# Performance work log

Hardware: AMD Instinct MI355X
Metric: run time of the kernel (lower is better)

Reference implementation:

```python
import jax, jax.numpy as jnp
import numpy as np

K = 5        # spline kernel_size per dim (dim=2 -> 25 kernel weights)
NPG = 75     # MNIST superpixel nodes per graph


def _spline_conv(x, src, dst, pseudo, emask, W, root, bias):
    """SplineConv, dim=2, kernel_size=5, degree=1 open splines, aggr='mean'.
    emask in {0,1} masks out coalesced-away (duplicate/self-loop) edges."""
    n = x.shape[0]
    v = jnp.clip(pseudo, 0.0, 1.0) * (K - 1)
    bot = jnp.clip(jnp.floor(v), 0, K - 2)
    frac = v - bot                                   # [E,2]
    bot = bot.astype(jnp.int32)
    xj = x[src] * emask[:, None]                     # [E,Fin] gathered source feats
    # aggregate-then-transform: acc[k,i,:] = sum over edges into i with basis k
    acc = jnp.zeros((K * K, n, x.shape[1]), x.dtype)
    for o0 in (0, 1):
        for o1 in (0, 1):
            w = (frac[:, 0] if o0 else 1.0 - frac[:, 0]) * (frac[:, 1] if o1 else 1.0 - frac[:, 1])
            kk = (bot[:, 0] + o0) + K * (bot[:, 1] + o1)
            acc = acc.at[kk, dst].add(w[:, None] * xj)
    out = jnp.einsum('knf,kfo->no', acc, W)
    deg = jax.ops.segment_sum(emask, dst, num_segments=n)
    return out / jnp.maximum(deg, 1.0)[:, None] + x @ root + bias


def _pool(x, pos, valid, batch, src, dst, emask, size, G, B):
    """voxel_grid + max_pool with static shapes: S=B*G*G clusters, masked."""
    S = B * G * G
    c = jnp.clip(jnp.floor(pos / size).astype(jnp.int32), 0, G - 1)
    cl = batch * (G * G) + c[:, 1] * G + c[:, 0]
    xm = jnp.where(valid[:, None] > 0, x, -1e30)
    px = jax.ops.segment_max(xm, cl, num_segments=S)
    cnt = jax.ops.segment_sum(valid, cl, num_segments=S)
    sval = (cnt > 0).astype(x.dtype)
    px = jnp.where(sval[:, None] > 0, px, 0.0)
    ppos = jax.ops.segment_sum(pos * valid[:, None], cl, num_segments=S) / jnp.maximum(cnt, 1.0)[:, None]
    nb = jnp.arange(S, dtype=jnp.int32) // (G * G)
    # remap edges to clusters; mask self loops and duplicates (= coalesce)
    nsrc, ndst = cl[src], cl[dst]
    m = (emask > 0) & (nsrc != ndst)
    a0 = jnp.where(m, nsrc, S)
    b0 = jnp.where(m, ndst, S)
    order = jnp.lexsort((b0, a0))
    a, b = a0[order], b0[order]
    first = jnp.concatenate([jnp.array([True]), (a[1:] != a[:-1]) | (b[1:] != b[:-1])])
    keep = jnp.zeros(src.shape[0], dtype=bool).at[order].set(first & (a < S))
    kf = keep.astype(x.dtype)
    # T.Cartesian(cat=False, norm=True): pseudo = (pos_src-pos_dst)/(2*max|.|)+0.5
    cart = ppos[nsrc] - ppos[ndst]
    amax = jnp.maximum(jnp.max(jnp.abs(cart) * kf[:, None]), 1e-12)
    pseudo = cart / (2.0 * amax) + 0.5
    return px, ppos, sval, nb, nsrc, ndst, kf, pseudo


def _forward(x, pos, src, dst, W1, r1, b1, W2, r2, b2, W3, r3, b3, fw1, fb1, fw2, fb2):
    N = x.shape[0]
    B = N // NPG
    batch = jnp.arange(N, dtype=jnp.int32) // NPG
    valid = jnp.ones((N,), x.dtype)
    emask = jnp.ones((src.shape[0],), x.dtype)
    cart = pos[src] - pos[dst]
    pseudo = cart / (2.0 * jnp.maximum(jnp.max(jnp.abs(cart)), 1e-12)) + 0.5
    x = jax.nn.elu(_spline_conv(x, src, dst, pseudo, emask, W1, r1, b1))
    x, pos, valid, batch, src, dst, emask, pseudo = _pool(x, pos, valid, batch, src, dst, emask, 5.0, 6, B)
    x = jax.nn.elu(_spline_conv(x, src, dst, pseudo, emask, W2, r2, b2))
    x, pos, valid, batch, src, dst, emask, pseudo = _pool(x, pos, valid, batch, src, dst, emask, 7.0, 5, B)
    x = jax.nn.elu(_spline_conv(x, src, dst, pseudo, emask, W3, r3, b3))
    # max_pool_x(cluster, x, batch, size=4): 2x2 voxel grid (size=14, end=27.99)
    c = jnp.clip(jnp.floor(pos / 14.0).astype(jnp.int32), 0, 1)
    cl = batch * 4 + c[:, 1] * 2 + c[:, 0]
    xm = jnp.where(valid[:, None] > 0, x, -1e30)
    px = jax.ops.segment_max(xm, cl, num_segments=B * 4)
    cnt = jax.ops.segment_sum(valid, cl, num_segments=B * 4)
    px = jnp.where((cnt > 0)[:, None], px, 0.0)
    h = jax.nn.elu(px.reshape(B, 4 * 64) @ fw1.T + fb1)
    logits = h @ fw2.T + fb2  # F.dropout is identity in eval mode
    return jax.nn.log_softmax(logits, axis=1)


def setup_inputs() -> dict:
    key = jax.random.key(0)
    ks = jax.random.split(key, 16)
    B, EPG = 1024, 1392
    N = B * NPG
    x = jax.random.normal(ks[0], (N, 1), jnp.float32)
    pos = jax.random.uniform(ks[1], (N, 2), jnp.float32) * 27.99
    s = jax.random.randint(ks[2], (B, EPG), 0, NPG)
    d = (s + 1 + jax.random.randint(ks[3], (B, EPG), 0, NPG - 1)) % NPG  # no self loops
    off = (jnp.arange(B, dtype=jnp.int32) * NPG)[:, None]
    src = (s + off).reshape(-1)
    dst = (d + off).reshape(-1)
    rn = lambda k, sh, sc: jax.random.normal(k, sh, jnp.float32) * sc
    return dict(x=x, pos=pos, src=src, dst=dst,
                W1=rn(ks[4], (25, 1, 32), 0.2), r1=rn(ks[5], (1, 32), 0.2), b1=jnp.zeros((32,), jnp.float32),
                W2=rn(ks[6], (25, 32, 64), 0.05), r2=rn(ks[7], (32, 64), 0.1), b2=jnp.zeros((64,), jnp.float32),
                W3=rn(ks[8], (25, 64, 64), 0.04), r3=rn(ks[9], (64, 64), 0.08), b3=jnp.zeros((64,), jnp.float32),
                fw1=rn(ks[10], (128, 256), 0.06), fb1=jnp.zeros((128,), jnp.float32),
                fw2=rn(ks[11], (10, 128), 0.09), fb2=jnp.zeros((10,), jnp.float32))


def reference(x, pos, src, dst, W1, r1, b1, W2, r2, b2, W3, r3, b3, fw1, fb1, fw2, fb2):
    return _forward(x, pos, src, dst, W1, r1, b1, W2, r2, b2, W3, r3, b3, fw1, fb1, fw2, fb2)
```

## Files before the change

kernel.cpp:

```cpp
#include <hip/hip_runtime.h>
#include <math.h>

#define NPG 75
#define KDIM 5

typedef _Float16 half8 __attribute__((ext_vector_type(8)));
typedef _Float16 half4 __attribute__((ext_vector_type(4)));
typedef float f32x4 __attribute__((ext_vector_type(4)));

__device__ __forceinline__ float eluf(float v){ return v > 0.f ? v : expf(v) - 1.f; }

__device__ __forceinline__ void atomAddF(float* p, float v){ unsafeAtomicAdd(p, v); }

__device__ __forceinline__ unsigned fenc(float f){
    unsigned u = __float_as_uint(f);
    return (u & 0x80000000u) ? ~u : (u | 0x80000000u);
}
__device__ __forceinline__ float fdec(unsigned u){
    return (u & 0x80000000u) ? __uint_as_float(u & 0x7FFFFFFFu) : __uint_as_float(~u);
}

__device__ __forceinline__ void fma25(float (&r)[25], const float (&wx)[5], const float (&wyx)[5]){
    #pragma unroll
    for (int b1 = 0; b1 < 5; b1++)
        #pragma unroll
        for (int b0 = 0; b0 < 5; b0++)
            asm("v_fmac_f32 %0, %1, %2" : "+v"(r[b1 * 5 + b0]) : "v"(wx[b0]), "v"(wyx[b1]));
}

__device__ __forceinline__ void spline2(float c0, float c1, float am, int* kks, float* wsp){
    float denom = 2.f * fmaxf(am, 1e-12f);
    float p0 = c0 / denom + 0.5f;
    float p1 = c1 / denom + 0.5f;
    p0 = fminf(fmaxf(p0, 0.f), 1.f) * 4.f;
    p1 = fminf(fmaxf(p1, 0.f), 1.f) * 4.f;
    float b0 = fminf(floorf(p0), 3.f);
    float b1 = fminf(floorf(p1), 3.f);
    float f0 = p0 - b0, f1 = p1 - b1;
    int i0 = (int)b0, i1 = (int)b1;
    wsp[0] = (1.f - f0) * (1.f - f1); kks[0] = i0     + KDIM *  i1;
    wsp[1] =        f0  * (1.f - f1); kks[1] = i0 + 1 + KDIM *  i1;
    wsp[2] = (1.f - f0) *        f1 ; kks[2] = i0     + KDIM * (i1 + 1);
    wsp[3] =        f0  *        f1 ; kks[3] = i0 + 1 + KDIM * (i1 + 1);
}

__global__ __launch_bounds__(256) void amax0_k(
        const float* __restrict__ pos, const int* __restrict__ src,
        const int* __restrict__ dst, int E4, unsigned* __restrict__ outbits){
    float cand = 0.f;
    for (int i = blockIdx.x * 256 + threadIdx.x; i < E4; i += gridDim.x * 256){
        int4 s4 = ((const int4*)src)[i];
        int4 d4 = ((const int4*)dst)[i];
        #pragma unroll
        for (int k = 0; k < 4; k++){
            int s = (&s4.x)[k], d = (&d4.x)[k];
            float c0 = pos[s*2]   - pos[d*2];
            float c1 = pos[s*2+1] - pos[d*2+1];
            cand = fmaxf(cand, fmaxf(fabsf(c0), fabsf(c1)));
        }
    }
    __shared__ float sm[256];
    sm[threadIdx.x] = cand; __syncthreads();
    for (int o = 128; o > 0; o >>= 1){
        if (threadIdx.x < o) sm[threadIdx.x] = fmaxf(sm[threadIdx.x], sm[threadIdx.x + o]);
        __syncthreads();
    }
    if (threadIdx.x == 0) atomicMax(outbits, __float_as_uint(sm[0]));
}

__global__ __launch_bounds__(512) void conv1dedup_k(
        const float* __restrict__ x, const float* __restrict__ pos,
        const int* __restrict__ src, const int* __restrict__ dst, int EPG,
        const unsigned* __restrict__ amaxp,
        const float* __restrict__ W1, const float* __restrict__ r1, const float* __restrict__ b1,
        float* __restrict__ px1, float* __restrict__ pp1, float* __restrict__ sv1,
        int* __restrict__ easrc, float2* __restrict__ ecart,
        int* __restrict__ rowptr2, int* __restrict__ kcnt, unsigned* __restrict__ amaxbits){
    __shared__ __align__(16) float acc[NPG * 28];
    __shared__ float deg[NPG];
    __shared__ float xl[NPG], p0l[NPG], p1l[NPG];
    __shared__ int   cli[NPG];
    __shared__ float W1s[800], r1s[32], b1s[32];
    __shared__ unsigned px[36 * 32];
    __shared__ float cnt[36], ps[72], ppS[72];
    __shared__ unsigned pm[36 * 36];
    __shared__ float degs[36];
    __shared__ int rs[37], cur[36];
    __shared__ float red[8];
    __shared__ unsigned short sdS[2048];

    const int b = blockIdx.x, t = threadIdx.x;
    const int lane = t & 63, wid = t >> 6;
    const int n0 = b * NPG, e0 = b * EPG;

    const float am = __uint_as_float(*amaxp);

    for (int i = t; i < NPG * 28; i += 512) acc[i] = 0.f;
    for (int i = t; i < 36 * 32; i += 512) px[i] = 0u;
    for (int i = t; i < 36 * 36; i += 512) pm[i] = 0xFFFFFFFFu;
    if (t < NPG) deg[t] = 0.f;
    if (t < 36){ cnt[t] = 0.f; degs[t] = 0.f; }
    if (t < 72) ps[t] = 0.f;
    for (int i = t; i < 800; i += 512) W1s[i] = W1[i];
    if (t < 32){ r1s[t] = r1[t]; b1s[t] = b1[t]; }
    if (t < NPG){
        float p0 = pos[(n0 + t) * 2], p1 = pos[(n0 + t) * 2 + 1];
        xl[t] = x[n0 + t]; p0l[t] = p0; p1l[t] = p1;
        int c0 = min(max((int)floorf(p0 / 5.f), 0), 5);
        int c1 = min(max((int)floorf(p1 / 5.f), 0), 5);
        cli[t] = c1 * 6 + c0;
    }
    __syncthreads();

    if (t < NPG){
        int c = cli[t];
        atomAddF(&cnt[c], 1.f);
        atomAddF(&ps[c*2],     p0l[t]);
        atomAddF(&ps[c*2 + 1], p1l[t]);
    }
    #pragma unroll 4
    for (int it = 0; it < 4; it++){
        int e = t + it * 512;
        if (e < EPG){
            int s = src[e0 + e] - n0;
            int d = dst[e0 + e] - n0;
            sdS[e] = (unsigned short)(s | (d << 8));
            float c0 = p0l[s] - p0l[d];
            float c1 = p1l[s] - p1l[d];
            int kks[4]; float wsp[4];
            spline2(c0, c1, am, kks, wsp);
            float xv = xl[s];
            #pragma unroll
            for (int c = 0; c < 4; c++) atomAddF(&acc[d*28 + kks[c]], wsp[c] * xv);
            atomAddF(&deg[d], 1.f);
        }
    }
    __syncthreads();

    if (t < 36){
        float c = cnt[t], m = fmaxf(c, 1.f);
        float q0 = ps[t*2] / m, q1 = ps[t*2 + 1] / m;
        ppS[t*2] = q0; ppS[t*2 + 1] = q1;
        pp1[(b*36 + t)*2]     = q0;
        pp1[(b*36 + t)*2 + 1] = q1;
        sv1[b*36 + t] = (c > 0.f) ? 1.f : 0.f;
    }
    {
        const int o = t & 31;
        float wreg[25];
        #pragma unroll
        for (int k = 0; k < 25; k++) wreg[k] = W1s[k * 32 + o];
        const float rro = r1s[o], bbo = b1s[o];
        const int ii = t >> 5;
        #pragma unroll
        for (int r = 0; r < 5; r++){
            int i = ii + r * 16;
            if (i < NPG){
                const float4* ar = (const float4*)(acc + i * 28);
                float s = 0.f;
                #pragma unroll
                for (int q = 0; q < 7; q++){
                    float4 aq = ar[q];
                    s += aq.x * wreg[q*4];
                    if (q*4 + 1 < 25) s += aq.y * wreg[q*4 + 1];
                    if (q*4 + 2 < 25) s += aq.z * wreg[q*4 + 2];
                    if (q*4 + 3 < 25) s += aq.w * wreg[q*4 + 3];
                }
                float v = s / fmaxf(deg[i], 1.f) + xl[i] * rro + bbo;
                v = eluf(v);
                atomicMax(&px[cli[i]*32 + o], fenc(v));
            }
        }
    }
    int lab[4];
    #pragma unroll 4
    for (int it = 0; it < 4; it++){
        int e = t + it * 512;
        lab[it] = 0;
        if (e < EPG){
            int sd = (int)sdS[e];
            int a  = cli[sd & 255];
            int bb = cli[sd >> 8];
            lab[it] = a | (bb << 8) | ((a != bb) ? 0x10000 : 0);
            if (a != bb) atomicMin(&pm[a * 36 + bb], (unsigned)e);
        }
    }
    __syncthreads();

    for (int idx = t; idx < 36 * 32; idx += 512){
        int s_ = idx >> 5;
        px1[(size_t)(b*36)*32 + idx] = (cnt[s_] > 0.f) ? fdec(px[idx]) : 0.f;
    }
    float cand = 0.f;
    unsigned keptM = 0;
    #pragma unroll 4
    for (int it = 0; it < 4; it++){
        int e = t + it * 512;
        int L = lab[it];
        if (L & 0x10000){
            int a = L & 255, bb = (L >> 8) & 255;
            if (pm[a * 36 + bb] == (unsigned)e){
                keptM |= 1u << it;
                atomAddF(&degs[bb], 1.f);
                float c0 = ppS[a*2]     - ppS[bb*2];
                float c1 = ppS[a*2 + 1] - ppS[bb*2 + 1];
                cand = fmaxf(cand, fmaxf(fabsf(c0), fabsf(c1)));
            }
        }
    }
    #pragma unroll
    for (int o = 1; o < 64; o <<= 1) cand = fmaxf(cand, __shfl_xor(cand, o, 64));
    if (lane == 0) red[wid] = cand;
    __syncthreads();
    if (t == 0){
        float m = red[0];
        #pragma unroll
        for (int i = 1; i < 8; i++) m = fmaxf(m, red[i]);
        atomicMax(amaxbits, __float_as_uint(m));
    }
    if (t < 64){
        int v = (t < 36) ? (int)degs[t] : 0;
        int incl = v;
        #pragma unroll
        for (int o = 1; o < 64; o <<= 1){
            int u = __shfl_up(incl, o, 64);
            if (t >= o) incl += u;
        }
        if (t == 0) rs[0] = 0;
        if (t < 36) rs[t + 1] = incl;
    }
    __syncthreads();
    if (t < 36){
        rowptr2[(b*36 + t)*2]     = e0 + rs[t];
        rowptr2[(b*36 + t)*2 + 1] = e0 + rs[t + 1];
        cur[t] = rs[t];
    }
    if (t == 0) kcnt[b] = rs[36];
    __syncthreads();
    #pragma unroll 4
    for (int it = 0; it < 4; it++){
        if (keptM & (1u << it)){
            int L = lab[it];
            int a = L & 255, bb = (L >> 8) & 255;
            int slot = atomicAdd(&cur[bb], 1);
            easrc[e0 + slot] = b*36 + a;
            ecart[e0 + slot] = make_float2(ppS[a*2] - ppS[bb*2], ppS[a*2 + 1] - ppS[bb*2 + 1]);
        }
    }
}

__global__ __launch_bounds__(1024) void dedup_pool_k(
        const int* __restrict__ easrc_in, const int* __restrict__ rowptr_in,
        const int* __restrict__ kcnt_in,
        const float* __restrict__ xin,
        const float* __restrict__ pp1, const float* __restrict__ sv1,
        int EPG,
        float* __restrict__ px2, float* __restrict__ pp2, float* __restrict__ sv2,
        int* __restrict__ easrc, float2* __restrict__ ecart,
        int* __restrict__ rowptr2, int* __restrict__ kcnt, unsigned* __restrict__ amaxbits){
    constexpr int GG = 25, NN = 36;
    __shared__ unsigned pm[GG * GG];
    __shared__ float degs[GG];
    __shared__ int rs[GG + 1];
    __shared__ int cur[GG];
    __shared__ float red[16];
    __shared__ int   clS[NN];
    __shared__ int   vld[NN];
    __shared__ int   rsS[NN + 1];
    __shared__ float ppS[2 * GG];
    __shared__ unsigned px[GG * 64];
    __shared__ float cnt[GG], ps[2 * GG];
    __shared__ unsigned short abS[1280];

    const int b = blockIdx.x, t = threadIdx.x;
    const int lane = t & 63, wid = t >> 6;
    const int e0 = b * EPG;
    const int cb25 = b * GG;
    const int nb36 = b * NN;

    for (int i = t; i < GG * GG; i += 1024) pm[i] = 0xFFFFFFFFu;
    for (int i = t; i < GG * 64; i += 1024) px[i] = 0u;
    if (t < GG){ degs[t] = 0.f; cnt[t] = 0.f; }
    if (t < 2 * GG) ps[t] = 0.f;
    if (t < NN){
        float v  = sv1[nb36 + t];
        float p0 = pp1[(nb36 + t)*2], p1 = pp1[(nb36 + t)*2 + 1];
        int c0 = min(max((int)floorf(p0 / 7.f), 0), 4);
        int c1 = min(max((int)floorf(p1 / 7.f), 0), 4);
        clS[t] = c1 * 5 + c0;
        vld[t] = (v > 0.f) ? 1 : 0;
        rsS[t] = rowptr_in[(nb36 + t)*2] - e0;
    }
    if (t == 0) rsS[NN] = kcnt_in[b];
    __syncthreads();

    const int kn = rsS[NN];

    if (t < NN && vld[t]){
        int c = clS[t];
        atomAddF(&cnt[c], 1.f);
        atomAddF(&ps[c*2],     pp1[(nb36 + t)*2]);
        atomAddF(&ps[c*2 + 1], pp1[(nb36 + t)*2 + 1]);
    }
    for (int idx = t; idx < NN * 64; idx += 1024){
        int i = idx >> 6, f = idx & 63;
        if (vld[i])
            atomicMax(&px[clS[i]*64 + f], fenc(xin[(size_t)(nb36 + i)*64 + f]));
    }
    #pragma unroll 2
    for (int it = 0; it < 2; it++){
        int s = t + it * 1024;
        if (s < kn){
            int r = 0;
            while (r < NN - 1 && rsS[r + 1] <= s) r++;
            int a2 = clS[easrc_in[e0 + s] - nb36];
            int b2 = clS[r];
            abS[s] = (unsigned short)(a2 | (b2 << 8) | ((a2 != b2) ? 0x8000 : 0));
            if (a2 != b2) atomicMin(&pm[a2 * GG + b2], (unsigned)s);
        }
    }
    __syncthreads();

    if (t < GG){
        float c = cnt[t], m = fmaxf(c, 1.f);
        float q0 = ps[t*2] / m, q1 = ps[t*2 + 1] / m;
        ppS[t*2] = q0; ppS[t*2 + 1] = q1;
        pp2[(cb25 + t)*2]     = q0;
        pp2[(cb25 + t)*2 + 1] = q1;
        sv2[cb25 + t] = (c > 0.f) ? 1.f : 0.f;
    }
    for (int idx = t; idx < GG * 64; idx += 1024){
        int s_ = idx >> 6;
        px2[(size_t)cb25*64 + idx] = (cnt[s_] > 0.f) ? fdec(px[idx]) : 0.f;
    }
    __syncthreads();

    float cand = 0.f;
    #pragma unroll 2
    for (int it = 0; it < 2; it++){
        int s = t + it * 1024;
        if (s < kn){
            int A = (int)abS[s];
            if (A & 0x8000){
                int a2 = A & 255, b2 = (A >> 8) & 127;
                if (pm[a2 * GG + b2] == (unsigned)s){
                    atomAddF(&degs[b2], 1.f);
                    float c0 = ppS[a2*2]     - ppS[b2*2];
                    float c1 = ppS[a2*2 + 1] - ppS[b2*2 + 1];
                    cand = fmaxf(cand, fmaxf(fabsf(c0), fabsf(c1)));
                }
            }
        }
    }
    #pragma unroll
    for (int o = 1; o < 64; o <<= 1) cand = fmaxf(cand, __shfl_xor(cand, o, 64));
    if (lane == 0) red[wid] = cand;
    __syncthreads();
    if (t == 0){
        float m = red[0];
        #pragma unroll
        for (int i = 1; i < 16; i++) m = fmaxf(m, red[i]);
        atomicMax(amaxbits, __float_as_uint(m));
    }
    if (t < 64){
        int v = (t < GG) ? (int)degs[t] : 0;
        int incl = v;
        #pragma unroll
        for (int o = 1; o < 64; o <<= 1){
            int u = __shfl_up(incl, o, 64);
            if (t >= o) incl += u;
        }
        if (t == 0) rs[0] = 0;
        if (t < GG) rs[t + 1] = incl;
    }
    __syncthreads();
    if (t < GG){
        rowptr2[(cb25 + t)*2]     = e0 + rs[t];
        rowptr2[(cb25 + t)*2 + 1] = e0 + rs[t + 1];
        cur[t] = rs[t];
    }
    if (t == 0) kcnt[b] = rs[GG];
    __syncthreads();
    #pragma unroll 2
    for (int it = 0; it < 2; it++){
        int s = t + it * 1024;
        if (s < kn){
            int A = (int)abS[s];
            if (A & 0x8000){
                int a2 = A & 255, b2 = (A >> 8) & 127;
                if (pm[a2 * GG + b2] == (unsigned)s){
                    int slot = atomicAdd(&cur[b2], 1);
                    easrc[e0 + slot] = cb25 + a2;
                    ecart[e0 + slot] = make_float2(ppS[a2*2] - ppS[b2*2], ppS[a2*2 + 1] - ppS[b2*2 + 1]);
                }
            }
        }
    }
}

__global__ void wswz2_k(const float* __restrict__ W2, const float* __restrict__ r2,
                        const float* __restrict__ W3, const float* __restrict__ r3,
                        _Float16* __restrict__ Wz2, _Float16* __restrict__ Wz3){
    int gid = blockIdx.x * 256 + threadIdx.x;
    const int T2 = 26 * 32 * 64;
    const int T3 = 26 * 64 * 64;
    const float* W; const float* root; _Float16* Wz; int FIN; int g;
    if (gid < T2){ W = W2; root = r2; Wz = Wz2; FIN = 32; g = gid; }
    else if (gid < T2 + T3){ W = W3; root = r3; Wz = Wz3; FIN = 64; g = gid - T2; }
    else return;
    int k = g >> 6, n = g & 63;
    float v = (k < 25 * FIN) ? W[(size_t)k * 64 + n] : root[(size_t)(k - 25 * FIN) * 64 + n];
    int kt = k >> 5, kr = k & 31, quad = kr >> 3, j = kr & 7;
    int lane = (quad << 4) | (n & 15);
    int nt = n >> 4;
    Wz[(((size_t)(kt * 4 + nt) * 64 + lane) << 3) + j] = (_Float16)v;
}

template<int FIN>
__global__ __launch_bounds__(256) void conv_gather_k(
        const float* __restrict__ x, const int* __restrict__ easrc,
        const float2* __restrict__ ecart, const unsigned* __restrict__ amaxp,
        const int* __restrict__ rowptr2, _Float16* __restrict__ Aout){
    constexpr int KTOT = 26 * FIN;
    __shared__ __align__(16) float pay[4][36][8];
    __shared__ int asrcS[4][36];
    const int w = threadIdx.x >> 6, lane = threadIdx.x & 63;
    const int node = blockIdx.x * 4 + w;
    const int row0 = rowptr2[node*2], row1 = rowptr2[node*2 + 1];
    const int ne = row1 - row0;
    constexpr int STEP = (FIN == 32) ? 2 : 1;
    const int sub = (FIN == 32) ? (lane >> 5) : 0;
    const int f = lane & (FIN - 1);

    if (lane < ne){
        int i = row0 + lane;
        float2 c = ecart[i];
        float am = __uint_as_float(*amaxp);
        float denom = 2.f * fmaxf(am, 1e-12f);
        float p0 = fminf(fmaxf(c.x / denom + 0.5f, 0.f), 1.f) * 4.f;
        float p1 = fminf(fmaxf(c.y / denom + 0.5f, 0.f), 1.f) * 4.f;
        float b0 = fminf(floorf(p0), 3.f);
        float b1 = fminf(floorf(p1), 3.f);
        int i0 = (int)b0, i1 = (int)b1;
        float f0 = p0 - b0, f1 = p1 - b1;
        float* d = &pay[w][lane][0];
        #pragma unroll
        for (int k = 0; k < 4; k++){
            d[k]     = (k == i0) ? (1.f - f0) : ((k == i0 + 1) ? f0 : 0.f);
            d[4 + k] = (k == i1) ? (1.f - f1) : ((k == i1 + 1) ? f1 : 0.f);
        }
        asrcS[w][lane] = easrc[i];
    }

    float r[25];
    #pragma unroll
    for (int b = 0; b < 25; b++) r[b] = 0.f;

    int j = sub;
    int aNext = 0;
    float xvCur = 0.f;
    if (j < ne){
        int aCur = asrcS[w][j];
        xvCur = x[(size_t)aCur * FIN + f];
        int j1 = (j + STEP < ne) ? j + STEP : j;
        aNext = asrcS[w][j1];
    }
    for (; j < ne; j += STEP){
        int jN  = j + STEP;
        int jNs = (jN < ne) ? jN : j;
        int jN2 = (jN + STEP < ne) ? jN + STEP : jNs;
        float xvN = x[(size_t)aNext * FIN + f];
        int aN2 = asrcS[w][jN2];
        float4 wa = *(const float4*)&pay[w][j][0];
        float4 wb = *(const float4*)&pay[w][j][4];
        float wx4 = 1.f - (wa.x + wa.y + wa.z + wa.w);
        float wy4 = 1.f - (wb.x + wb.y + wb.z + wb.w);
        float wx[5]  = {wa.x, wa.y, wa.z, wa.w, wx4};
        float wyx[5] = {wb.x * xvCur, wb.y * xvCur, wb.z * xvCur, wb.w * xvCur, wy4 * xvCur};
        fma25(r, wx, wyx);
        xvCur = xvN; aNext = aN2;
    }

    if (FIN == 32){
        #pragma unroll
        for (int b = 0; b < 25; b++) r[b] += __shfl_xor(r[b], 32, 64);
    }

    float inv = 1.f / (float)max(ne, 1);
    _Float16* dstrow = Aout + (size_t)node * KTOT;
    if (FIN == 64){
        #pragma unroll
        for (int b = 0; b < 25; b++) dstrow[b * 64 + f] = (_Float16)(r[b] * inv);
        dstrow[25 * 64 + f] = (_Float16)x[(size_t)node * 64 + f];
    } else {
        #pragma unroll
        for (int b = 0; b < 25; b++)
            if ((b & 1) == sub) dstrow[b * 32 + f] = (_Float16)(r[b] * inv);
        if (sub == 0) dstrow[25 * 32 + f] = (_Float16)x[(size_t)node * 32 + f];
    }
}

template<int KTOT>
__global__ __launch_bounds__(256) void conv_mfma_k(
        const _Float16* __restrict__ A, const _Float16* __restrict__ Wz,
        const float* __restrict__ bias, int M, float* __restrict__ out){
    constexpr int NSTEP = KTOT / 32;
    const int w = threadIdx.x >> 6, lane = threadIdx.x & 63;
    const int m0 = blockIdx.x * 64 + w * 16;
    const int quad = lane >> 4;

    f32x4 acc[4];
    #pragma unroll
    for (int nt = 0; nt < 4; nt++) acc[nt] = (f32x4){0.f, 0.f, 0.f, 0.f};

    const half8* __restrict__ Arow = (const half8*)(A + (size_t)(m0 + (lane & 15)) * KTOT);
    const half8* __restrict__ Wp   = (const half8*)Wz + lane;

    for (int kt = 0; kt < NSTEP; kt++){
        half8 a = Arow[kt * 4 + quad];
        #pragma unroll
        for (int nt = 0; nt < 4; nt++){
            half8 b = Wp[(kt * 4 + nt) * 64];
            acc[nt] = __builtin_amdgcn_mfma_f32_16x16x32_f16(a, b, acc[nt], 0, 0, 0);
        }
    }

    float* cp = out + (size_t)m0 * 64;
    const int r = quad * 4, c = lane & 15;
    #pragma unroll
    for (int nt = 0; nt < 4; nt++){
        float bv = bias[nt * 16 + c];
        #pragma unroll
        for (int i = 0; i < 4; i++)
            cp[(size_t)(r + i) * 64 + nt * 16 + c] = eluf(acc[nt][i] + bv);
    }
}

__global__ __launch_bounds__(256) void final_k(
        const float* __restrict__ xin, const float* __restrict__ ppin,
        const float* __restrict__ svin,
        const float* __restrict__ fw1, const float* __restrict__ fb1,
        const float* __restrict__ fw2, const float* __restrict__ fb2,
        float* __restrict__ out){
    __shared__ unsigned px[4 * 64];
    __shared__ float cnt[4];
    __shared__ int cli[25];
    __shared__ float xr[256];
    __shared__ float h[128];
    __shared__ float lg[10];
    __shared__ float lse;
    const int b = blockIdx.x, t = threadIdx.x;

    if (t < 4*64) px[t] = 0u;
    if (t < 4) cnt[t] = 0.f;
    if (t < 25){
        float v  = svin[b*25 + t];
        float p0 = ppin[(b*25 + t)*2], p1 = ppin[(b*25 + t)*2 + 1];
        int c0 = min(max((int)floorf(p0 / 14.f), 0), 1);
        int c1 = min(max((int)floorf(p1 / 14.f), 0), 1);
        int c = c1 * 2 + c0;
        cli[t] = (v > 0.f) ? c : -1;
    }
    __syncthreads();
    if (t < 25 && cli[t] >= 0) atomAddF(&cnt[cli[t]], 1.f);
    __syncthreads();
    for (int idx = t; idx < 25 * 64; idx += 256){
        int i = idx >> 6, f = idx & 63;
        if (cli[i] >= 0)
            atomicMax(&px[cli[i]*64 + f], fenc(xin[(size_t)(b*25 + i)*64 + f]));
    }
    __syncthreads();
    xr[t] = (cnt[t >> 6] > 0.f) ? fdec(px[t]) : 0.f;
    __syncthreads();
    if (t < 128){
        float s = fb1[t];
        const float4* wrow = (const float4*)(fw1 + (size_t)t * 256);
        #pragma unroll 4
        for (int i = 0; i < 64; i++){
            float4 q = wrow[i];
            s += xr[i*4]   * q.x;
            s += xr[i*4+1] * q.y;
            s += xr[i*4+2] * q.z;
            s += xr[i*4+3] * q.w;
        }
        h[t] = eluf(s);
    }
    __syncthreads();
    if (t < 10){
        float s2 = fb2[t];
        const float* w2 = fw2 + (size_t)t * 128;
        for (int j = 0; j < 128; j++) s2 += h[j] * w2[j];
        lg[t] = s2;
    }
    __syncthreads();
    if (t == 0){
        float m = lg[0];
        for (int c = 1; c < 10; c++) m = fmaxf(m, lg[c]);
        float se = 0.f;
        for (int c = 0; c < 10; c++) se += expf(lg[c] - m);
        lse = m + logf(se);
    }
    __syncthreads();
    if (t < 10) out[(size_t)b*10 + t] = lg[t] - lse;
}

extern "C" void kernel_launch(void* const* d_in, const int* in_sizes, int n_in,
                              void* d_out, int out_size, void* d_ws, size_t ws_size,
                              hipStream_t stream) {
    const float* x   = (const float*)d_in[0];
    const float* pos = (const float*)d_in[1];
    const int*   src = (const int*)d_in[2];
    const int*   dst = (const int*)d_in[3];
    const float* W1  = (const float*)d_in[4];
    const float* r1  = (const float*)d_in[5];
    const float* b1  = (const float*)d_in[6];
    const float* W2  = (const float*)d_in[7];
    const float* r2  = (const float*)d_in[8];
    const float* b2  = (const float*)d_in[9];
    const float* W3  = (const float*)d_in[10];
    const float* r3  = (const float*)d_in[11];
    const float* b3  = (const float*)d_in[12];
    const float* fw1 = (const float*)d_in[13];
    const float* fb1 = (const float*)d_in[14];
    const float* fw2 = (const float*)d_in[15];
    const float* fb2 = (const float*)d_in[16];
    float* out = (float*)d_out;

    const int N   = in_sizes[0];
    const int E   = in_sizes[2];
    const int B   = N / NPG;
    const int EPG = E / B;
    const int S1  = B * 36;
    const int S2  = B * 25;

    float* w = (float*)d_ws;
    size_t off = 0;
    auto alloc = [&](size_t nelem){ size_t o = off; off += (nelem + 63) & ~(size_t)63; return o; };

    size_t o_scal = alloc(4);
    size_t o_px1  = alloc((size_t)S1 * 32);
    size_t o_pp1  = alloc((size_t)S1 * 2);
    size_t o_sv1  = alloc(S1);
    size_t o_easrc= alloc(E);
    size_t o_ecart= alloc((size_t)2 * E);
    size_t o_kcnt = alloc(B);
    size_t o_rp2  = alloc((size_t)2 * S1);
    size_t o_rp3  = alloc((size_t)2 * S2);
    size_t o_out2 = alloc((size_t)S1 * 64);
    size_t o_px2  = alloc((size_t)S2 * 64);
    size_t o_pp2  = alloc((size_t)S2 * 2);
    size_t o_sv2  = alloc(S2);
    size_t o_out3 = alloc((size_t)S2 * 64);
    size_t o_wz2  = alloc((size_t)26 * 32 * 64 / 2 + 64);
    size_t o_wz3  = alloc((size_t)26 * 64 * 64 / 2 + 64);
    size_t accAhalfs = (size_t)S1 * 832 > (size_t)S2 * 1664 ? (size_t)S1 * 832 : (size_t)S2 * 1664;
    size_t o_accA = alloc((accAhalfs + 1) / 2);

    hipMemsetAsync(w + o_scal, 0, 4 * sizeof(float), stream);

    unsigned* scal = (unsigned*)(w + o_scal);
    _Float16* Wz2  = (_Float16*)(w + o_wz2);
    _Float16* Wz3  = (_Float16*)(w + o_wz3);
    _Float16* A16  = (_Float16*)(w + o_accA);
    auto nb = [](long long t){ return (unsigned)((t + 255) / 256); };

    wswz2_k<<<nb(26 * 32 * 64 + 26 * 64 * 64), 256, 0, stream>>>(W2, r2, W3, r3, Wz2, Wz3);

    const int E4 = E / 4;
    int gA = (E4 + 255) / 256; if (gA > 512) gA = 512;
    amax0_k<<<gA, 256, 0, stream>>>(pos, src, dst, E4, scal + 0);

    conv1dedup_k<<<B, 512, 0, stream>>>(x, pos, src, dst, EPG, scal + 0, W1, r1, b1,
                                        w + o_px1, w + o_pp1, w + o_sv1,
                                        (int*)(w + o_easrc), (float2*)(w + o_ecart),
                                        (int*)(w + o_rp2), (int*)(w + o_kcnt), scal + 1);

    conv_gather_k<32><<<S1 / 4, 256, 0, stream>>>(
        w + o_px1, (int*)(w + o_easrc), (const float2*)(w + o_ecart), scal + 1,
        (int*)(w + o_rp2), A16);
    conv_mfma_k<832><<<S1 / 64, 256, 0, stream>>>(A16, Wz2, b2, S1, w + o_out2);

    dedup_pool_k<<<B, 1024, 0, stream>>>(
        (int*)(w + o_easrc), (int*)(w + o_rp2), (int*)(w + o_kcnt),
        w + o_out2, w + o_pp1, w + o_sv1, EPG,
        w + o_px2, w + o_pp2, w + o_sv2,
        (int*)(w + o_easrc), (float2*)(w + o_ecart),
        (int*)(w + o_rp3), (int*)(w + o_kcnt), scal + 2);

    conv_gather_k<64><<<S2 / 4, 256, 0, stream>>>(
        w + o_px2, (int*)(w + o_easrc), (const float2*)(w + o_ecart), scal + 2,
        (int*)(w + o_rp3), A16);
    conv_mfma_k<1664><<<S2 / 64, 256, 0, stream>>>(A16, Wz3, b3, S2, w + o_out3);

    final_k<<<B, 256, 0, stream>>>(w + o_out3, w + o_pp2, w + o_sv2,
                                   fw1, fb1, fw2, fb2, out);
}
```

Measured before the change: 320.7 us.

## Fuse spline gather and MFMA GEMM into single kernels per conv layer

Merges the per-node spline aggregation kernel and the fp16 MFMA transform kernel into one kernel per conv layer. The aggregated A rows are staged in padded LDS instead of a global fp16 buffer, which removes a global write/read round trip and one launch per layer. Conv3 splits the K dimension across two wave groups and reduces their partial sums through shared memory. In exchange, the large LDS footprint and 32-node blocks lower occupancy and change how the grid parallelism is spread.

```diff
diff --git a/kernel.cpp b/kernel.cpp
--- a/kernel.cpp
+++ b/kernel.cpp
@@ -5,7 +5,6 @@
 #define KDIM 5
 
 typedef _Float16 half8 __attribute__((ext_vector_type(8)));
-typedef _Float16 half4 __attribute__((ext_vector_type(4)));
 typedef float f32x4 __attribute__((ext_vector_type(4)));
 
 __device__ __forceinline__ float eluf(float v){ return v > 0.f ? v : expf(v) - 1.f; }
@@ -42,6 +41,20 @@
     wsp[1] =        f0  * (1.f - f1); kks[1] = i0 + 1 + KDIM *  i1;
     wsp[2] = (1.f - f0) *        f1 ; kks[2] = i0     + KDIM * (i1 + 1);
     wsp[3] =        f0  *        f1 ; kks[3] = i0 + 1 + KDIM * (i1 + 1);
+}
+
+__device__ __forceinline__ void spline_pay(float2 c, float denom, float* d){
+    float p0 = fminf(fmaxf(c.x / denom + 0.5f, 0.f), 1.f) * 4.f;
+    float p1 = fminf(fmaxf(c.y / denom + 0.5f, 0.f), 1.f) * 4.f;
+    float b0 = fminf(floorf(p0), 3.f);
+    float b1 = fminf(floorf(p1), 3.f);
+    int i0 = (int)b0, i1 = (int)b1;
+    float f0 = p0 - b0, f1 = p1 - b1;
+    #pragma unroll
+    for (int k = 0; k < 4; k++){
+        d[k]     = (k == i0) ? (1.f - f0) : ((k == i0 + 1) ? f0 : 0.f);
+        d[4 + k] = (k == i1) ? (1.f - f1) : ((k == i1 + 1) ? f1 : 0.f);
+    }
 }
 
 __global__ __launch_bounds__(256) void amax0_k(
@@ -416,123 +429,181 @@
     Wz[(((size_t)(kt * 4 + nt) * 64 + lane) << 3) + j] = (_Float16)v;
 }
 
-template<int FIN>
-__global__ __launch_bounds__(256) void conv_gather_k(
+__global__ __launch_bounds__(512) void conv2f_k(
         const float* __restrict__ x, const int* __restrict__ easrc,
         const float2* __restrict__ ecart, const unsigned* __restrict__ amaxp,
-        const int* __restrict__ rowptr2, _Float16* __restrict__ Aout){
-    constexpr int KTOT = 26 * FIN;
-    __shared__ __align__(16) float pay[4][36][8];
-    __shared__ int asrcS[4][36];
+        const int* __restrict__ rowptr2, const _Float16* __restrict__ Wz,
+        const float* __restrict__ bias, float* __restrict__ out){
+    constexpr int PAD = 840;
+    __shared__ __align__(16) _Float16 Alds[32 * PAD];
+    __shared__ __align__(16) float pay[8][36][8];
+    __shared__ int asrcS[8][36];
+
     const int w = threadIdx.x >> 6, lane = threadIdx.x & 63;
-    const int node = blockIdx.x * 4 + w;
-    const int row0 = rowptr2[node*2], row1 = rowptr2[node*2 + 1];
-    const int ne = row1 - row0;
-    constexpr int STEP = (FIN == 32) ? 2 : 1;
-    const int sub = (FIN == 32) ? (lane >> 5) : 0;
-    const int f = lane & (FIN - 1);
-
-    if (lane < ne){
-        int i = row0 + lane;
-        float2 c = ecart[i];
-        float am = __uint_as_float(*amaxp);
-        float denom = 2.f * fmaxf(am, 1e-12f);
-        float p0 = fminf(fmaxf(c.x / denom + 0.5f, 0.f), 1.f) * 4.f;
-        float p1 = fminf(fmaxf(c.y / denom + 0.5f, 0.f), 1.f) * 4.f;
-        float b0 = fminf(floorf(p0), 3.f);
-        float b1 = fminf(floorf(p1), 3.f);
-        int i0 = (int)b0, i1 = (int)b1;
-        float f0 = p0 - b0, f1 = p1 - b1;
-        float* d = &pay[w][lane][0];
-        #pragma unroll
-        for (int k = 0; k < 4; k++){
-            d[k]     = (k == i0) ? (1.f - f0) : ((k == i0 + 1) ? f0 : 0.f);
-            d[4 + k] = (k == i1) ? (1.f - f1) : ((k == i1 + 1) ? f1 : 0.f);
-        }
-        asrcS[w][lane] = easrc[i];
-    }
-
-    float r[25];
+    const int sub = lane >> 5, f = lane & 31;
+    const float am = __uint_as_float(*amaxp);
+    const float denom = 2.f * fmaxf(am, 1e-12f);
+
     #pragma unroll
-    for (int b = 0; b < 25; b++) r[b] = 0.f;
-
-    int j = sub;
-    int aNext = 0;
-    float xvCur = 0.f;
-    if (j < ne){
-        int aCur = asrcS[w][j];
-        xvCur = x[(size_t)aCur * FIN + f];
-        int j1 = (j + STEP < ne) ? j + STEP : j;
-        aNext = asrcS[w][j1];
-    }
-    for (; j < ne; j += STEP){
-        int jN  = j + STEP;
-        int jNs = (jN < ne) ? jN : j;
-        int jN2 = (jN + STEP < ne) ? jN + STEP : jNs;
-        float xvN = x[(size_t)aNext * FIN + f];
-        int aN2 = asrcS[w][jN2];
-        float4 wa = *(const float4*)&pay[w][j][0];
-        float4 wb = *(const float4*)&pay[w][j][4];
-        float wx4 = 1.f - (wa.x + wa.y + wa.z + wa.w);
-        float wy4 = 1.f - (wb.x + wb.y + wb.z + wb.w);
-        float wx[5]  = {wa.x, wa.y, wa.z, wa.w, wx4};
-        float wyx[5] = {wb.x * xvCur, wb.y * xvCur, wb.z * xvCur, wb.w * xvCur, wy4 * xvCur};
-        fma25(r, wx, wyx);
-        xvCur = xvN; aNext = aN2;
-    }
-
-    if (FIN == 32){
+    for (int i = 0; i < 4; i++){
+        const int nloc = w * 4 + i;
+        const int node = blockIdx.x * 32 + nloc;
+        const int row0 = rowptr2[node*2], row1 = rowptr2[node*2 + 1];
+        const int ne = row1 - row0;
+
+        if (lane < ne){
+            spline_pay(ecart[row0 + lane], denom, &pay[w][lane][0]);
+            asrcS[w][lane] = easrc[row0 + lane];
+        }
+
+        float r[25];
+        #pragma unroll
+        for (int b = 0; b < 25; b++) r[b] = 0.f;
+
+        int j = sub;
+        int aNext = 0;
+        float xvCur = 0.f;
+        if (j < ne){
+            int aCur = asrcS[w][j];
+            xvCur = x[(size_t)aCur * 32 + f];
+            int j1 = (j + 2 < ne) ? j + 2 : j;
+            aNext = asrcS[w][j1];
+        }
+        for (; j < ne; j += 2){
+            int jN  = j + 2;
+            int jNs = (jN < ne) ? jN : j;
+            int jN2 = (jN + 2 < ne) ? jN + 2 : jNs;
+            float xvN = x[(size_t)aNext * 32 + f];
+            int aN2 = asrcS[w][jN2];
+            float4 wa = *(const float4*)&pay[w][j][0];
+            float4 wb = *(const float4*)&pay[w][j][4];
+            float wx4 = 1.f - (wa.x + wa.y + wa.z + wa.w);
+            float wy4 = 1.f - (wb.x + wb.y + wb.z + wb.w);
+            float wx[5]  = {wa.x, wa.y, wa.z, wa.w, wx4};
+            float wyx[5] = {wb.x * xvCur, wb.y * xvCur, wb.z * xvCur, wb.w * xvCur, wy4 * xvCur};
+            fma25(r, wx, wyx);
+            xvCur = xvN; aNext = aN2;
+        }
         #pragma unroll
         for (int b = 0; b < 25; b++) r[b] += __shfl_xor(r[b], 32, 64);
-    }
-
-    float inv = 1.f / (float)max(ne, 1);
-    _Float16* dstrow = Aout + (size_t)node * KTOT;
-    if (FIN == 64){
-        #pragma unroll
-        for (int b = 0; b < 25; b++) dstrow[b * 64 + f] = (_Float16)(r[b] * inv);
-        dstrow[25 * 64 + f] = (_Float16)x[(size_t)node * 64 + f];
-    } else {
+
+        float inv = 1.f / (float)max(ne, 1);
+        _Float16* dstrow = &Alds[nloc * PAD];
         #pragma unroll
         for (int b = 0; b < 25; b++)
             if ((b & 1) == sub) dstrow[b * 32 + f] = (_Float16)(r[b] * inv);
         if (sub == 0) dstrow[25 * 32 + f] = (_Float16)x[(size_t)node * 32 + f];
     }
-}
-
-template<int KTOT>
-__global__ __launch_bounds__(256) void conv_mfma_k(
-        const _Float16* __restrict__ A, const _Float16* __restrict__ Wz,
-        const float* __restrict__ bias, int M, float* __restrict__ out){
-    constexpr int NSTEP = KTOT / 32;
+    __syncthreads();
+
+    const int mt = w >> 2, nt = w & 3;
+    const int quad = lane >> 4, mr = lane & 15;
+    f32x4 acc = (f32x4){0.f, 0.f, 0.f, 0.f};
+    const _Float16* arow = &Alds[(mt * 16 + mr) * PAD];
+    const half8* __restrict__ Wp = (const half8*)Wz + lane;
+    for (int kt = 0; kt < 26; kt++){
+        half8 a = *(const half8*)(arow + kt * 32 + quad * 8);
+        half8 b = Wp[(kt * 4 + nt) * 64];
+        acc = __builtin_amdgcn_mfma_f32_16x16x32_f16(a, b, acc, 0, 0, 0);
+    }
+    float* cp = out + (size_t)(blockIdx.x * 32 + mt * 16) * 64;
+    const int r_ = quad * 4, c_ = lane & 15;
+    float bv = bias[nt * 16 + c_];
+    #pragma unroll
+    for (int i = 0; i < 4; i++)
+        cp[(size_t)(r_ + i) * 64 + nt * 16 + c_] = eluf(acc[i] + bv);
+}
+
+__global__ __launch_bounds__(1024) void conv3f_k(
+        const float* __restrict__ x, const int* __restrict__ easrc,
+        const float2* __restrict__ ecart, const unsigned* __restrict__ amaxp,
+        const int* __restrict__ rowptr2, const _Float16* __restrict__ Wz,
+        const float* __restrict__ bias, float* __restrict__ out){
+    constexpr int PAD = 1672;
+    __shared__ __align__(16) _Float16 Alds[32 * PAD];
+    __shared__ __align__(16) float scratchF[3456];
+    __shared__ int asrcS[16][24];
+
     const int w = threadIdx.x >> 6, lane = threadIdx.x & 63;
-    const int m0 = blockIdx.x * 64 + w * 16;
-    const int quad = lane >> 4;
-
-    f32x4 acc[4];
+    const float am = __uint_as_float(*amaxp);
+    const float denom = 2.f * fmaxf(am, 1e-12f);
+    float* payW = scratchF + w * 24 * 8;
+
     #pragma unroll
-    for (int nt = 0; nt < 4; nt++) acc[nt] = (f32x4){0.f, 0.f, 0.f, 0.f};
-
-    const half8* __restrict__ Arow = (const half8*)(A + (size_t)(m0 + (lane & 15)) * KTOT);
-    const half8* __restrict__ Wp   = (const half8*)Wz + lane;
-
-    for (int kt = 0; kt < NSTEP; kt++){
-        half8 a = Arow[kt * 4 + quad];
-        #pragma unroll
-        for (int nt = 0; nt < 4; nt++){
-            half8 b = Wp[(kt * 4 + nt) * 64];
-            acc[nt] = __builtin_amdgcn_mfma_f32_16x16x32_f16(a, b, acc[nt], 0, 0, 0);
-        }
-    }
-
-    float* cp = out + (size_t)m0 * 64;
-    const int r = quad * 4, c = lane & 15;
-    #pragma unroll
-    for (int nt = 0; nt < 4; nt++){
-        float bv = bias[nt * 16 + c];
+    for (int i = 0; i < 2; i++){
+        const int nloc = w * 2 + i;
+        const int node = blockIdx.x * 32 + nloc;
+        const int row0 = rowptr2[node*2], row1 = rowptr2[node*2 + 1];
+        const int ne = row1 - row0;
+
+        if (lane < ne){
+            spline_pay(ecart[row0 + lane], denom, payW + lane * 8);
+            asrcS[w][lane] = easrc[row0 + lane];
+        }
+
+        float r[25];
+        #pragma unroll
+        for (int b = 0; b < 25; b++) r[b] = 0.f;
+
+        int j = 0;
+        int aNext = 0;
+        float xvCur = 0.f;
+        if (j < ne){
+            int aCur = asrcS[w][j];
+            xvCur = x[(size_t)aCur * 64 + lane];
+            int j1 = (1 < ne) ? 1 : 0;
+            aNext = asrcS[w][j1];
+        }
+        for (; j < ne; j++){
+            int jN  = j + 1;
+            int jNs = (jN < ne) ? jN : j;
+            int jN2 = (jN + 1 < ne) ? jN + 1 : jNs;
+            float xvN = x[(size_t)aNext * 64 + lane];
+            int aN2 = asrcS[w][jN2];
+            float4 wa = *(const float4*)(payW + j * 8);
+            float4 wb = *(const float4*)(payW + j * 8 + 4);
+            float wx4 = 1.f - (wa.x + wa.y + wa.z + wa.w);
+            float wy4 = 1.f - (wb.x + wb.y + wb.z + wb.w);
+            float wx[5]  = {wa.x, wa.y, wa.z, wa.w, wx4};
+            float wyx[5] = {wb.x * xvCur, wb.y * xvCur, wb.z * xvCur, wb.w * xvCur, wy4 * xvCur};
+            fma25(r, wx, wyx);
+            xvCur = xvN; aNext = aN2;
+        }
+
+        float inv = 1.f / (float)max(ne, 1);
+        _Float16* dstrow = &Alds[nloc * PAD];
+        #pragma unroll
+        for (int b = 0; b < 25; b++) dstrow[b * 64 + lane] = (_Float16)(r[b] * inv);
+        dstrow[25 * 64 + lane] = (_Float16)x[(size_t)node * 64 + lane];
+    }
+    __syncthreads();
+
+    const int tile = w & 7, khalf = w >> 3;
+    const int mt = tile >> 2, nt = tile & 3;
+    const int quad = lane >> 4, mr = lane & 15;
+    f32x4 acc = (f32x4){0.f, 0.f, 0.f, 0.f};
+    const _Float16* arow = &Alds[(mt * 16 + mr) * PAD];
+    const half8* __restrict__ Wp = (const half8*)Wz + lane;
+    const int kt0 = khalf * 26;
+    for (int kt = 0; kt < 26; kt++){
+        half8 a = *(const half8*)(arow + (kt0 + kt) * 32 + quad * 8);
+        half8 b = Wp[((kt0 + kt) * 4 + nt) * 64];
+        acc = __builtin_amdgcn_mfma_f32_16x16x32_f16(a, b, acc, 0, 0, 0);
+    }
+    const int r_ = quad * 4, c_ = lane & 15;
+    if (khalf == 1){
+        float* Cp = scratchF + tile * 256;
+        #pragma unroll
+        for (int i = 0; i < 4; i++) Cp[(r_ + i) * 16 + c_] = acc[i];
+    }
+    __syncthreads();
+    if (khalf == 0){
+        const float* Cp = scratchF + tile * 256;
+        float* cp = out + (size_t)(blockIdx.x * 32 + mt * 16) * 64;
+        float bv = bias[nt * 16 + c_];
         #pragma unroll
         for (int i = 0; i < 4; i++)
-            cp[(size_t)(r + i) * 64 + nt * 16 + c] = eluf(acc[nt][i] + bv);
+            cp[(size_t)(r_ + i) * 64 + nt * 16 + c_] = eluf(acc[i] + Cp[(r_ + i) * 16 + c_] + bv);
     }
 }
 
@@ -653,15 +724,12 @@
     size_t o_out3 = alloc((size_t)S2 * 64);
     size_t o_wz2  = alloc((size_t)26 * 32 * 64 / 2 + 64);
     size_t o_wz3  = alloc((size_t)26 * 64 * 64 / 2 + 64);
-    size_t accAhalfs = (size_t)S1 * 832 > (size_t)S2 * 1664 ? (size_t)S1 * 832 : (size_t)S2 * 1664;
-    size_t o_accA = alloc((accAhalfs + 1) / 2);
 
     hipMemsetAsync(w + o_scal, 0, 4 * sizeof(float), stream);
 
     unsigned* scal = (unsigned*)(w + o_scal);
     _Float16* Wz2  = (_Float16*)(w + o_wz2);
     _Float16* Wz3  = (_Float16*)(w + o_wz3);
-    _Float16* A16  = (_Float16*)(w + o_accA);
     auto nb = [](long long t){ return (unsigned)((t + 255) / 256); };
 
     wswz2_k<<<nb(26 * 32 * 64 + 26 * 64 * 64), 256, 0, stream>>>(W2, r2, W3, r3, Wz2, Wz3);
@@ -675,10 +743,9 @@
                                         (int*)(w + o_easrc), (float2*)(w + o_ecart),
                                         (int*)(w + o_rp2), (int*)(w + o_kcnt), scal + 1);
 
-    conv_gather_k<32><<<S1 / 4, 256, 0, stream>>>(
+    conv2f_k<<<S1 / 32, 512, 0, stream>>>(
         w + o_px1, (int*)(w + o_easrc), (const float2*)(w + o_ecart), scal + 1,
-        (int*)(w + o_rp2), A16);
-    conv_mfma_k<832><<<S1 / 64, 256, 0, stream>>>(A16, Wz2, b2, S1, w + o_out2);
+        (int*)(w + o_rp2), Wz2, b2, w + o_out2);
 
     dedup_pool_k<<<B, 1024, 0, stream>>>(
         (int*)(w + o_easrc), (int*)(w + o_rp2), (int*)(w + o_kcnt),
@@ -687,10 +754,9 @@
         (int*)(w + o_easrc), (float2*)(w + o_ecart),
         (int*)(w + o_rp3), (int*)(w + o_kcnt), scal + 2);
 
-    conv_gather_k<64><<<S2 / 4, 256, 0, stream>>>(
+    conv3f_k<<<S2 / 32, 1024, 0, stream>>>(
         w + o_px2, (int*)(w + o_easrc), (const float2*)(w + o_ecart), scal + 2,
-        (int*)(w + o_rp3), A16);
-    conv_mfma_k<1664><<<S2 / 64, 256, 0, stream>>>(A16, Wz3, b3, S2, w + o_out3);
+        (int*)(w + o_rp3), Wz3, b3, w + o_out3);
 
     final_k<<<B, 256, 0, stream>>>(w + o_out3, w + o_pp2, w + o_sv2,
                                    fw1, fb1, fw2, fb2, out);
```

Result: slower. 327.2 us (+2.0%).
